# Optimization experiments

Measured on AMD Instinct MI355X. Metric: run time of the kernel, lower is better.

Reference implementation:

```python
import jax, jax.numpy as jnp
import numpy as np

NUM_USERS = 100_000
NUM_ITEMS = 50_000
D = 64           # input_dim
K = 3            # num_weights (basis diagonal weights)
C = 5            # num_classes
E = 2_000_000    # number of (user, item) edges


def setup_inputs() -> dict:
    key = jax.random.key(0)
    ks = jax.random.split(key, 8)
    he = np.sqrt(2.0 / D).astype(np.float32)  # he_normal scale for [*, D] weights
    return {
        "u_feat": jax.random.normal(ks[0], (NUM_USERS, D), dtype=jnp.float32),
        "v_feat": jax.random.normal(ks[1], (NUM_ITEMS, D), dtype=jnp.float32),
        "W": jax.random.normal(ks[2], (K, D), dtype=jnp.float32) * he,
        "scalars": jax.random.normal(ks[3], (K, C), dtype=jnp.float32) * np.sqrt(2.0 / K).astype(np.float32),
        "u_bias": jnp.zeros((NUM_USERS, C), dtype=jnp.float32) + 0.01 * jax.random.normal(ks[4], (NUM_USERS, C), dtype=jnp.float32),
        "v_bias": jnp.zeros((NUM_ITEMS, C), dtype=jnp.float32) + 0.01 * jax.random.normal(ks[5], (NUM_ITEMS, C), dtype=jnp.float32),
        "u_idx": jax.random.randint(ks[6], (E,), 0, NUM_USERS, dtype=jnp.int32),
        "v_idx": jax.random.randint(ks[7], (E,), 0, NUM_ITEMS, dtype=jnp.int32),
    }


def reference(u_feat, v_feat, W, scalars, u_bias, v_bias, u_idx, v_idx):
    # Gather per-edge user/item embedding rows: [E, D]
    u_g = u_feat[u_idx]
    v_g = v_feat[v_idx]
    # Diagonal bilinear form per basis k: sum_d u_d * W[k,d] * v_d
    # = (u * v) @ W^T  -> basis_outputs: [E, K]
    basis_outputs = (u_g * v_g) @ W.T
    # Combine bases into class logits: [E, C]
    outputs = basis_outputs @ scalars
    # user_item_bias=True: add gathered per-user / per-item class biases
    outputs = outputs + u_bias[u_idx] + v_bias[v_idx]
    # activation=None -> linear
    return outputs
```

## Files before the change

### kernel.cpp

```cpp
#include <hip/hip_runtime.h>
#include <hip/hip_fp16.h>


template <int CTRL>
__device__ __forceinline__ float dpp_add(float x) {
    int t = __builtin_amdgcn_update_dpp(0, __float_as_int(x), CTRL, 0xF, 0xF, true);
    return x + __int_as_float(t);
}

__device__ __forceinline__ void reduce16_3(float& a, float& b, float& c) {
    a = dpp_add<0xB1>(a);  b = dpp_add<0xB1>(b);  c = dpp_add<0xB1>(c);
    a = dpp_add<0x4E>(a);  b = dpp_add<0x4E>(b);  c = dpp_add<0x4E>(c);
    a = dpp_add<0x124>(a); b = dpp_add<0x124>(b); c = dpp_add<0x124>(c);
    a = dpp_add<0x128>(a); b = dpp_add<0x128>(b); c = dpp_add<0x128>(c);
}

__global__ __launch_bounds__(256) void convert_tables_fp16(
    const float* __restrict__ u_feat, const float* __restrict__ v_feat,
    __half* __restrict__ u_h, __half* __restrict__ v_h, int nu, int nv)
{
    const int tid  = blockIdx.x * blockDim.x + threadIdx.x;
    const int nthr = gridDim.x * blockDim.x;
    for (int i = tid * 4; i < nu; i += nthr * 4) {
        const float4 x = *reinterpret_cast<const float4*>(u_feat + i);
        *reinterpret_cast<__half2*>(u_h + i)     = __floats2half2_rn(x.x, x.y);
        *reinterpret_cast<__half2*>(u_h + i + 2) = __floats2half2_rn(x.z, x.w);
    }
    for (int i = tid * 4; i < nv; i += nthr * 4) {
        const float4 x = *reinterpret_cast<const float4*>(v_feat + i);
        *reinterpret_cast<__half2*>(v_h + i)     = __floats2half2_rn(x.x, x.y);
        *reinterpret_cast<__half2*>(v_h + i + 2) = __floats2half2_rn(x.z, x.w);
    }
}

__global__ __launch_bounds__(256) void bilinear_edges_h(
    const __half* __restrict__ u_h, const __half* __restrict__ v_h,
    const float* __restrict__ W, const float* __restrict__ scalars,
    const float* __restrict__ u_bias, const float* __restrict__ v_bias,
    const int* __restrict__ u_idx, const int* __restrict__ v_idx,
    float* __restrict__ out, int E)
{
    const int tid    = blockIdx.x * blockDim.x + threadIdx.x;
    const int sl     = threadIdx.x & 15;
    const int group  = tid >> 4;
    const int ngroup = (gridDim.x * blockDim.x) >> 4;
    const int step   = ngroup * 2;

    const int d0 = sl * 4;
    float w0[4], w1[4], w2[4];
    #pragma unroll
    for (int j = 0; j < 4; ++j) {
        w0[j] = W[0 * 64 + d0 + j];
        w1[j] = W[1 * 64 + d0 + j];
        w2[j] = W[2 * 64 + d0 + j];
    }
    float s0 = 0.f, s1 = 0.f, s2 = 0.f;
    if (sl < 5) { s0 = scalars[0 * 5 + sl]; s1 = scalars[1 * 5 + sl]; s2 = scalars[2 * 5 + sl]; }

    int e0 = group * 2;
    if (e0 >= E) return;

    int uu0 = u_idx[e0];
    int vv0 = v_idx[e0];
    int uu1 = (e0 + 1 < E) ? u_idx[e0 + 1] : uu0;
    int vv1 = (e0 + 1 < E) ? v_idx[e0 + 1] : vv0;

    for (; e0 < E; e0 += step) {
        const int  e1   = e0 + 1;
        const bool has1 = (e1 < E);
        const int cu0 = uu0, cv0 = vv0, cu1 = uu1, cv1 = vv1;

        const float2 ur0 = *reinterpret_cast<const float2*>(u_h + (size_t)cu0 * 64 + d0);
        const float2 vr0 = *reinterpret_cast<const float2*>(v_h + (size_t)cv0 * 64 + d0);
        const float2 ur1 = *reinterpret_cast<const float2*>(u_h + (size_t)cu1 * 64 + d0);
        const float2 vr1 = *reinterpret_cast<const float2*>(v_h + (size_t)cv1 * 64 + d0);

        const int en = e0 + step;
        if (en < E) {
            uu0 = u_idx[en];
            vv0 = v_idx[en];
            const int en1 = en + 1;
            uu1 = (en1 < E) ? u_idx[en1] : uu0;
            vv1 = (en1 < E) ? v_idx[en1] : vv0;
        }

        float ub0 = 0.f, vb0 = 0.f, ub1 = 0.f, vb1 = 0.f;
        if (sl < 5) {
            ub0 = u_bias[(size_t)cu0 * 5 + sl];
            vb0 = v_bias[(size_t)cv0 * 5 + sl];
            ub1 = u_bias[(size_t)cu1 * 5 + sl];
            vb1 = v_bias[(size_t)cv1 * 5 + sl];
        }

        const float2 u0a = __half22float2(*reinterpret_cast<const __half2*>(&ur0.x));
        const float2 u0b = __half22float2(*reinterpret_cast<const __half2*>(&ur0.y));
        const float2 v0a = __half22float2(*reinterpret_cast<const __half2*>(&vr0.x));
        const float2 v0b = __half22float2(*reinterpret_cast<const __half2*>(&vr0.y));
        const float2 u1a = __half22float2(*reinterpret_cast<const __half2*>(&ur1.x));
        const float2 u1b = __half22float2(*reinterpret_cast<const __half2*>(&ur1.y));
        const float2 v1a = __half22float2(*reinterpret_cast<const __half2*>(&vr1.x));
        const float2 v1b = __half22float2(*reinterpret_cast<const __half2*>(&vr1.y));

        const float a0 = u0a.x * v0a.x, a1 = u0a.y * v0a.y,
                    a2 = u0b.x * v0b.x, a3 = u0b.y * v0b.y;
        const float b0 = u1a.x * v1a.x, b1 = u1a.y * v1a.y,
                    b2 = u1b.x * v1b.x, b3 = u1b.y * v1b.y;

        float qa0 = a0*w0[0] + a1*w0[1] + a2*w0[2] + a3*w0[3];
        float qa1 = a0*w1[0] + a1*w1[1] + a2*w1[2] + a3*w1[3];
        float qa2 = a0*w2[0] + a1*w2[1] + a2*w2[2] + a3*w2[3];
        float qb0 = b0*w0[0] + b1*w0[1] + b2*w0[2] + b3*w0[3];
        float qb1 = b0*w1[0] + b1*w1[1] + b2*w1[2] + b3*w1[3];
        float qb2 = b0*w2[0] + b1*w2[1] + b2*w2[2] + b3*w2[3];

        reduce16_3(qa0, qa1, qa2);
        reduce16_3(qb0, qb1, qb2);

        if (sl < 5) {
            out[(size_t)e0 * 5 + sl] = qa0 * s0 + qa1 * s1 + qa2 * s2 + ub0 + vb0;
            if (has1)
                out[(size_t)e1 * 5 + sl] = qb0 * s0 + qb1 * s1 + qb2 * s2 + ub1 + vb1;
        }
    }
}

__global__ __launch_bounds__(256) void bilinear_edges_f32(
    const float* __restrict__ u_feat, const float* __restrict__ v_feat,
    const float* __restrict__ W, const float* __restrict__ scalars,
    const float* __restrict__ u_bias, const float* __restrict__ v_bias,
    const int* __restrict__ u_idx, const int* __restrict__ v_idx,
    float* __restrict__ out, int E)
{
    const int tid    = blockIdx.x * blockDim.x + threadIdx.x;
    const int sl     = threadIdx.x & 15;
    const int group  = tid >> 4;
    const int ngroup = (gridDim.x * blockDim.x) >> 4;

    const int d0 = sl * 4;
    float w0[4], w1[4], w2[4];
    #pragma unroll
    for (int j = 0; j < 4; ++j) {
        w0[j] = W[0 * 64 + d0 + j];
        w1[j] = W[1 * 64 + d0 + j];
        w2[j] = W[2 * 64 + d0 + j];
    }
    float s0 = 0.f, s1 = 0.f, s2 = 0.f;
    if (sl < 5) { s0 = scalars[0 * 5 + sl]; s1 = scalars[1 * 5 + sl]; s2 = scalars[2 * 5 + sl]; }

    for (int e = group; e < E; e += ngroup) {
        const int uu = u_idx[e];
        const int vv = v_idx[e];
        const float4 u4 = *reinterpret_cast<const float4*>(u_feat + (size_t)uu * 64 + d0);
        const float4 v4 = *reinterpret_cast<const float4*>(v_feat + (size_t)vv * 64 + d0);
        float ub = 0.f, vb = 0.f;
        if (sl < 5) { ub = u_bias[(size_t)uu * 5 + sl]; vb = v_bias[(size_t)vv * 5 + sl]; }

        const float p0 = u4.x * v4.x, p1 = u4.y * v4.y,
                    p2 = u4.z * v4.z, p3 = u4.w * v4.w;
        float q0 = p0*w0[0] + p1*w0[1] + p2*w0[2] + p3*w0[3];
        float q1 = p0*w1[0] + p1*w1[1] + p2*w1[2] + p3*w1[3];
        float q2 = p0*w2[0] + p1*w2[1] + p2*w2[2] + p3*w2[3];
        reduce16_3(q0, q1, q2);
        if (sl < 5)
            out[(size_t)e * 5 + sl] = q0 * s0 + q1 * s1 + q2 * s2 + ub + vb;
    }
}

extern "C" void kernel_launch(void* const* d_in, const int* in_sizes, int n_in,
                              void* d_out, int out_size, void* d_ws, size_t ws_size,
                              hipStream_t stream) {
    const float* u_feat  = (const float*)d_in[0];
    const float* v_feat  = (const float*)d_in[1];
    const float* W       = (const float*)d_in[2];
    const float* scalars = (const float*)d_in[3];
    const float* u_bias  = (const float*)d_in[4];
    const float* v_bias  = (const float*)d_in[5];
    const int*   u_idx   = (const int*)d_in[6];
    const int*   v_idx   = (const int*)d_in[7];
    float*       out     = (float*)d_out;

    const int nu = in_sizes[0];
    const int nv = in_sizes[1];
    const int E  = in_sizes[6];

    const size_t ws_need = (size_t)(nu + nv) * sizeof(__half);

    if (ws_size >= ws_need) {
        __half* u_h = (__half*)d_ws;
        __half* v_h = u_h + nu;
        convert_tables_fp16<<<2048, 256, 0, stream>>>(u_feat, v_feat, u_h, v_h, nu, nv);
        bilinear_edges_h<<<2048, 256, 0, stream>>>(
            u_h, v_h, W, scalars, u_bias, v_bias, u_idx, v_idx, out, E);
    } else {
        bilinear_edges_f32<<<2048, 256, 0, stream>>>(
            u_feat, v_feat, W, scalars, u_bias, v_bias, u_idx, v_idx, out, E);
    }
}
```

Before: 208.0 us.

## Compute edge logits with fp16 MFMA using a pre-folded W·scalars matrix

Replaces the per-edge DPP reduction kernel with a wave-level MFMA kernel. Each wave processes 16 edges at a time, multiplies gathered fp16 user and item rows elementwise in fp16, and runs two 16x16x32 MFMAs against a B matrix formed by folding W and scalars into one 64x5 fp16 matrix. This removes the cross-lane shuffle reductions and the separate combine step. In exchange, the elementwise product and the folded weights are now computed in fp16, which adds rounding error. Bias rows are gathered with a second load of the indices in the epilogue.

```diff
diff --git a/kernel.cpp b/kernel.cpp
--- a/kernel.cpp
+++ b/kernel.cpp
@@ -2,18 +2,8 @@
 #include <hip/hip_fp16.h>
 
 
-template <int CTRL>
-__device__ __forceinline__ float dpp_add(float x) {
-    int t = __builtin_amdgcn_update_dpp(0, __float_as_int(x), CTRL, 0xF, 0xF, true);
-    return x + __int_as_float(t);
-}
-
-__device__ __forceinline__ void reduce16_3(float& a, float& b, float& c) {
-    a = dpp_add<0xB1>(a);  b = dpp_add<0xB1>(b);  c = dpp_add<0xB1>(c);
-    a = dpp_add<0x4E>(a);  b = dpp_add<0x4E>(b);  c = dpp_add<0x4E>(c);
-    a = dpp_add<0x124>(a); b = dpp_add<0x124>(b); c = dpp_add<0x124>(c);
-    a = dpp_add<0x128>(a); b = dpp_add<0x128>(b); c = dpp_add<0x128>(c);
-}
+typedef _Float16 f16x8 __attribute__((ext_vector_type(8)));
+typedef float    f32x4 __attribute__((ext_vector_type(4)));
 
 __global__ __launch_bounds__(256) void convert_tables_fp16(
     const float* __restrict__ u_feat, const float* __restrict__ v_feat,
@@ -33,95 +23,73 @@
     }
 }
 
-__global__ __launch_bounds__(256) void bilinear_edges_h(
+__global__ __launch_bounds__(256) void bilinear_mfma(
     const __half* __restrict__ u_h, const __half* __restrict__ v_h,
     const float* __restrict__ W, const float* __restrict__ scalars,
     const float* __restrict__ u_bias, const float* __restrict__ v_bias,
     const int* __restrict__ u_idx, const int* __restrict__ v_idx,
-    float* __restrict__ out, int E)
+    float* __restrict__ out, int E, int ntiles)
 {
-    const int tid    = blockIdx.x * blockDim.x + threadIdx.x;
-    const int sl     = threadIdx.x & 15;
-    const int group  = tid >> 4;
-    const int ngroup = (gridDim.x * blockDim.x) >> 4;
-    const int step   = ngroup * 2;
+    const int lane = threadIdx.x & 63;
+    const int r    = lane & 15;
+    const int h    = lane >> 4;
+    const int w    = blockIdx.x * (blockDim.x >> 6) + (threadIdx.x >> 6);
+    const int nw   = gridDim.x * (blockDim.x >> 6);
 
-    const int d0 = sl * 4;
-    float w0[4], w1[4], w2[4];
+    float sc0 = 0.f, sc1 = 0.f, sc2 = 0.f;
+    if (r < 5) { sc0 = scalars[r]; sc1 = scalars[5 + r]; sc2 = scalars[10 + r]; }
+    f16x8 B0, B1;
     #pragma unroll
-    for (int j = 0; j < 4; ++j) {
-        w0[j] = W[0 * 64 + d0 + j];
-        w1[j] = W[1 * 64 + d0 + j];
-        w2[j] = W[2 * 64 + d0 + j];
+    for (int j = 0; j < 8; ++j) {
+        const int d0 = h * 8 + j;
+        const int d1 = 32 + d0;
+        B0[j] = (_Float16)(W[d0] * sc0 + W[64 + d0] * sc1 + W[128 + d0] * sc2);
+        B1[j] = (_Float16)(W[d1] * sc0 + W[64 + d1] * sc1 + W[128 + d1] * sc2);
     }
-    float s0 = 0.f, s1 = 0.f, s2 = 0.f;
-    if (sl < 5) { s0 = scalars[0 * 5 + sl]; s1 = scalars[1 * 5 + sl]; s2 = scalars[2 * 5 + sl]; }
 
-    int e0 = group * 2;
-    if (e0 >= E) return;
+    for (int t = w; t < ntiles; t += nw) {
+        const int e0 = t * 16;
+        const int er = min(e0 + r, E - 1);
+        const int ua = u_idx[er];
+        const int va = v_idx[er];
 
-    int uu0 = u_idx[e0];
-    int vv0 = v_idx[e0];
-    int uu1 = (e0 + 1 < E) ? u_idx[e0 + 1] : uu0;
-    int vv1 = (e0 + 1 < E) ? v_idx[e0 + 1] : vv0;
+        const __half* up = u_h + (size_t)ua * 64 + h * 8;
+        const __half* vp = v_h + (size_t)va * 64 + h * 8;
+        const f16x8 au0 = *reinterpret_cast<const f16x8*>(up);
+        const f16x8 au1 = *reinterpret_cast<const f16x8*>(up + 32);
+        const f16x8 av0 = *reinterpret_cast<const f16x8*>(vp);
+        const f16x8 av1 = *reinterpret_cast<const f16x8*>(vp + 32);
 
-    for (; e0 < E; e0 += step) {
-        const int  e1   = e0 + 1;
-        const bool has1 = (e1 < E);
-        const int cu0 = uu0, cv0 = vv0, cu1 = uu1, cv1 = vv1;
+        const f16x8 A0 = au0 * av0;
+        const f16x8 A1 = au1 * av1;
 
-        const float2 ur0 = *reinterpret_cast<const float2*>(u_h + (size_t)cu0 * 64 + d0);
-        const float2 vr0 = *reinterpret_cast<const float2*>(v_h + (size_t)cv0 * 64 + d0);
-        const float2 ur1 = *reinterpret_cast<const float2*>(u_h + (size_t)cu1 * 64 + d0);
-        const float2 vr1 = *reinterpret_cast<const float2*>(v_h + (size_t)cv1 * 64 + d0);
+        f32x4 acc = {0.f, 0.f, 0.f, 0.f};
+        acc = __builtin_amdgcn_mfma_f32_16x16x32_f16(A0, B0, acc, 0, 0, 0);
+        acc = __builtin_amdgcn_mfma_f32_16x16x32_f16(A1, B1, acc, 0, 0, 0);
 
-        const int en = e0 + step;
-        if (en < E) {
-            uu0 = u_idx[en];
-            vv0 = v_idx[en];
-            const int en1 = en + 1;
-            uu1 = (en1 < E) ? u_idx[en1] : uu0;
-            vv1 = (en1 < E) ? v_idx[en1] : vv0;
-        }
-
-        float ub0 = 0.f, vb0 = 0.f, ub1 = 0.f, vb1 = 0.f;
-        if (sl < 5) {
-            ub0 = u_bias[(size_t)cu0 * 5 + sl];
-            vb0 = v_bias[(size_t)cv0 * 5 + sl];
-            ub1 = u_bias[(size_t)cu1 * 5 + sl];
-            vb1 = v_bias[(size_t)cv1 * 5 + sl];
-        }
-
-        const float2 u0a = __half22float2(*reinterpret_cast<const __half2*>(&ur0.x));
-        const float2 u0b = __half22float2(*reinterpret_cast<const __half2*>(&ur0.y));
-        const float2 v0a = __half22float2(*reinterpret_cast<const __half2*>(&vr0.x));
-        const float2 v0b = __half22float2(*reinterpret_cast<const __half2*>(&vr0.y));
-        const float2 u1a = __half22float2(*reinterpret_cast<const __half2*>(&ur1.x));
-        const float2 u1b = __half22float2(*reinterpret_cast<const __half2*>(&ur1.y));
-        const float2 v1a = __half22float2(*reinterpret_cast<const __half2*>(&vr1.x));
-        const float2 v1b = __half22float2(*reinterpret_cast<const __half2*>(&vr1.y));
-
-        const float a0 = u0a.x * v0a.x, a1 = u0a.y * v0a.y,
-                    a2 = u0b.x * v0b.x, a3 = u0b.y * v0b.y;
-        const float b0 = u1a.x * v1a.x, b1 = u1a.y * v1a.y,
-                    b2 = u1b.x * v1b.x, b3 = u1b.y * v1b.y;
-
-        float qa0 = a0*w0[0] + a1*w0[1] + a2*w0[2] + a3*w0[3];
-        float qa1 = a0*w1[0] + a1*w1[1] + a2*w1[2] + a3*w1[3];
-        float qa2 = a0*w2[0] + a1*w2[1] + a2*w2[2] + a3*w2[3];
-        float qb0 = b0*w0[0] + b1*w0[1] + b2*w0[2] + b3*w0[3];
-        float qb1 = b0*w1[0] + b1*w1[1] + b2*w1[2] + b3*w1[3];
-        float qb2 = b0*w2[0] + b1*w2[1] + b2*w2[2] + b3*w2[3];
-
-        reduce16_3(qa0, qa1, qa2);
-        reduce16_3(qb0, qb1, qb2);
-
-        if (sl < 5) {
-            out[(size_t)e0 * 5 + sl] = qa0 * s0 + qa1 * s1 + qa2 * s2 + ub0 + vb0;
-            if (has1)
-                out[(size_t)e1 * 5 + sl] = qb0 * s0 + qb1 * s1 + qb2 * s2 + ub1 + vb1;
+        #pragma unroll
+        for (int i = 0; i < 4; ++i) {
+            const int e = e0 + h * 4 + i;
+            if (r < 5 && e < E) {
+                const int ui = u_idx[e];
+                const int vi = v_idx[e];
+                out[(size_t)e * 5 + r] =
+                    acc[i] + u_bias[(size_t)ui * 5 + r] + v_bias[(size_t)vi * 5 + r];
+            }
         }
     }
+}
+
+template <int CTRL>
+__device__ __forceinline__ float dpp_add(float x) {
+    int t = __builtin_amdgcn_update_dpp(0, __float_as_int(x), CTRL, 0xF, 0xF, true);
+    return x + __int_as_float(t);
+}
+__device__ __forceinline__ void reduce16_3(float& a, float& b, float& c) {
+    a = dpp_add<0xB1>(a);  b = dpp_add<0xB1>(b);  c = dpp_add<0xB1>(c);
+    a = dpp_add<0x4E>(a);  b = dpp_add<0x4E>(b);  c = dpp_add<0x4E>(c);
+    a = dpp_add<0x124>(a); b = dpp_add<0x124>(b); c = dpp_add<0x124>(c);
+    a = dpp_add<0x128>(a); b = dpp_add<0x128>(b); c = dpp_add<0x128>(c);
 }
 
 __global__ __launch_bounds__(256) void bilinear_edges_f32(
@@ -139,13 +107,13 @@
     const int d0 = sl * 4;
     float w0[4], w1[4], w2[4];
     #pragma unroll
-    for (int j = 0; j < 4; ++j) {
-        w0[j] = W[0 * 64 + d0 + j];
-        w1[j] = W[1 * 64 + d0 + j];
-        w2[j] = W[2 * 64 + d0 + j];
+    for (int t = 0; t < 4; ++t) {
+        w0[t] = W[0 * 64 + d0 + t];
+        w1[t] = W[1 * 64 + d0 + t];
+        w2[t] = W[2 * 64 + d0 + t];
     }
     float s0 = 0.f, s1 = 0.f, s2 = 0.f;
-    if (sl < 5) { s0 = scalars[0 * 5 + sl]; s1 = scalars[1 * 5 + sl]; s2 = scalars[2 * 5 + sl]; }
+    if (sl < 5) { s0 = scalars[sl]; s1 = scalars[5 + sl]; s2 = scalars[10 + sl]; }
 
     for (int e = group; e < E; e += ngroup) {
         const int uu = u_idx[e];
@@ -188,9 +156,10 @@
     if (ws_size >= ws_need) {
         __half* u_h = (__half*)d_ws;
         __half* v_h = u_h + nu;
+        const int ntiles = (E + 15) / 16;
         convert_tables_fp16<<<2048, 256, 0, stream>>>(u_feat, v_feat, u_h, v_h, nu, nv);
-        bilinear_edges_h<<<2048, 256, 0, stream>>>(
-            u_h, v_h, W, scalars, u_bias, v_bias, u_idx, v_idx, out, E);
+        bilinear_mfma<<<2048, 256, 0, stream>>>(
+            u_h, v_h, W, scalars, u_bias, v_bias, u_idx, v_idx, out, E, ntiles);
     } else {
         bilinear_edges_f32<<<2048, 256, 0, stream>>>(
             u_feat, v_feat, W, scalars, u_bias, v_bias, u_idx, v_idx, out, E);
```

Result: slower. 261.9 us (+25.9%).
